# Kernel optimization log

Measured on AMD Instinct MI355X. Metric: run time of the kernel, lower is better.

Reference implementation:

```python
import jax, jax.numpy as jnp
import numpy as np

NEG = -9e15

def setup_inputs() -> dict:
    key = jax.random.key(0)
    k_h, k_adj, k_W, k_bW, k_a1, k_b1, k_a2, k_b2 = jax.random.split(key, 8)
    N, IN, OUT = 8192, 512, 512
    h = jax.random.normal(k_h, (N, IN), dtype=jnp.float32)
    adj = jax.random.randint(k_adj, (N, N), 0, 2, dtype=jnp.int32)
    # torch Linear default init: U(-1/sqrt(fan_in), 1/sqrt(fan_in))
    s_in = 1.0 / np.sqrt(IN)
    s_out = 1.0 / np.sqrt(OUT)
    W = jax.random.uniform(k_W, (IN, OUT), minval=-s_in, maxval=s_in, dtype=jnp.float32)
    bW = jax.random.uniform(k_bW, (OUT,), minval=-s_in, maxval=s_in, dtype=jnp.float32)
    a1 = jax.random.uniform(k_a1, (OUT,), minval=-s_out, maxval=s_out, dtype=jnp.float32)
    b1 = jax.random.uniform(k_b1, (), minval=-s_out, maxval=s_out, dtype=jnp.float32)
    a2 = jax.random.uniform(k_a2, (OUT,), minval=-s_out, maxval=s_out, dtype=jnp.float32)
    b2 = jax.random.uniform(k_b2, (), minval=-s_out, maxval=s_out, dtype=jnp.float32)
    return {"h": h, "adj": adj, "W": W, "bW": bW, "a1": a1, "b1": b1, "a2": a2, "b2": b2}

def reference(h, adj, W, bW, a1, b1, a2, b2):
    alpha = 0.2
    # Wh: [N, OUT]; dropout is identity at inference (training=False)
    Wh = h @ W + bW
    Wha1 = Wh @ a1 + b1  # [N]
    Wha2 = Wh @ a2 + b2  # [N]
    e = Wha1[:, None] + Wha2[None, :]  # [N, N] broadcast additive scores
    e = jnp.where(e > 0, e, alpha * e)  # leaky relu
    e = jnp.where(adj > 0, e, jnp.float32(-9e15))
    attention = jax.nn.softmax(e, axis=1)
    h_prime = attention @ Wh  # [N, OUT]
    return h_prime
```

## Files before the change

kernel.cpp:

```cpp
#include <hip/hip_runtime.h>
#include <stdint.h>


#define NN 8192
#define DD 512

typedef __attribute__((ext_vector_type(8))) short short8;
typedef __attribute__((ext_vector_type(4))) float f32x4;
typedef __attribute__((ext_vector_type(4))) float float4v;
typedef __attribute__((ext_vector_type(4))) unsigned short ushort4v;

__device__ __forceinline__ uint16_t f2bf(float f) {
  union { float f; uint32_t u; } v; v.f = f;
  uint32_t u = v.u;
  u += 0x7fffu + ((u >> 16) & 1u);
  return (uint16_t)(u >> 16);
}
__device__ __forceinline__ float bf2f(uint16_t b) {
  union { uint32_t u; float f; } v; v.u = ((uint32_t)b) << 16;
  return v.f;
}

__device__ __forceinline__ void async_copy16(uint16_t* lds, const uint16_t* g) {
  __builtin_amdgcn_global_load_lds(
      (const __attribute__((address_space(1))) uint32_t*)g,
      (__attribute__((address_space(3))) uint32_t*)lds, 16, 0, 0);
}

__global__ __launch_bounds__(256) void conv_wt(const float* __restrict__ W,
                                               uint16_t* __restrict__ WT) {
  int idx = blockIdx.x * 256 + threadIdx.x;
  int k = idx >> 9, c = idx & 511;
  WT[c * 512 + k] = f2bf(W[idx]);
}

__global__ __launch_bounds__(512) void wh_gemm(const float* __restrict__ h,
                                               const uint16_t* __restrict__ WT,
                                               const float* __restrict__ bW,
                                               uint16_t* __restrict__ WhT) {
  __shared__ __align__(16) uint16_t At[32 * 32];
  __shared__ __align__(16) uint16_t Bt[512 * 32];
  int tid = threadIdx.x;
  int wave = tid >> 6, lane = tid & 63;
  int l15 = lane & 15, quad = lane >> 4;
  int i0 = blockIdx.x * 32;
  f32x4 acc[2][4] = {};
  for (int k0 = 0; k0 < 512; k0 += 32) {
    if (tid < 256) {
      int r = tid >> 3, ks = (tid & 7) * 4;
      float4v hv = *(const float4v*)(h + (size_t)(i0 + r) * 512 + k0 + ks);
      ushort4v p;
      p.x = f2bf(hv.x); p.y = f2bf(hv.y); p.z = f2bf(hv.z); p.w = f2bf(hv.w);
      *(ushort4v*)&At[r * 32 + ks] = p;
    }
    #pragma unroll
    for (int rr = 0; rr < 4; ++rr) {
      int idx = rr * 512 + tid;
      int c = idx >> 2, q = idx & 3;
      async_copy16(&Bt[idx * 8], WT + c * 512 + k0 + q * 8);
    }
    __syncthreads();
    short8 a0 = *(const short8*)&At[l15 * 32 + quad * 8];
    short8 a1f = *(const short8*)&At[(l15 + 16) * 32 + quad * 8];
    #pragma unroll
    for (int nt = 0; nt < 4; ++nt) {
      int c = wave * 64 + nt * 16 + l15;
      short8 b = *(const short8*)&Bt[c * 32 + quad * 8];
      acc[0][nt] = __builtin_amdgcn_mfma_f32_16x16x32_bf16(a0, b, acc[0][nt], 0, 0, 0);
      acc[1][nt] = __builtin_amdgcn_mfma_f32_16x16x32_bf16(a1f, b, acc[1][nt], 0, 0, 0);
    }
    __syncthreads();
  }
  #pragma unroll
  for (int mt = 0; mt < 2; ++mt) {
    int ib = i0 + mt * 16 + quad * 4;
    #pragma unroll
    for (int nt = 0; nt < 4; ++nt) {
      int c = wave * 64 + nt * 16 + l15;
      float bias = bW[c];
      ushort4v p;
      p.x = f2bf(acc[mt][nt].x + bias);
      p.y = f2bf(acc[mt][nt].y + bias);
      p.z = f2bf(acc[mt][nt].z + bias);
      p.w = f2bf(acc[mt][nt].w + bias);
      *(ushort4v*)&WhT[(size_t)c * 8192 + ib] = p;
    }
  }
}

__global__ __launch_bounds__(256) void zero_k(float* __restrict__ p) {
  p[blockIdx.x * 256 + threadIdx.x] = 0.f;
}

__global__ __launch_bounds__(256) void scores2(const uint16_t* __restrict__ WhT,
                                               const float* __restrict__ a1,
                                               const float* __restrict__ a2,
                                               float* __restrict__ s1,
                                               float* __restrict__ s2) {
  int cc = blockIdx.x >> 5;
  int ic = blockIdx.x & 31;
  int i = ic * 256 + threadIdx.x;
  float r1 = 0.f, r2 = 0.f;
  int cbase = cc * 128;
  #pragma unroll 8
  for (int c = cbase; c < cbase + 128; ++c) {
    float v = bf2f(WhT[(size_t)c * 8192 + i]);
    r1 = fmaf(v, a1[c], r1);
    r2 = fmaf(v, a2[c], r2);
  }
  atomicAdd(&s1[i], r1);
  atomicAdd(&s2[i], r2);
}

__global__ __launch_bounds__(256) void w_k(const int* __restrict__ adj,
                                           const float* __restrict__ s1,
                                           const float* __restrict__ s2,
                                           const float* __restrict__ b1,
                                           const float* __restrict__ b2,
                                           uint16_t* __restrict__ w,
                                           float* __restrict__ dinv) {
  __shared__ float wsum[4];
  int i = blockIdx.x;
  int tid = threadIdx.x;
  float base = s1[i] + b1[0] + b2[0];
  const int* arow = adj + (size_t)i * 8192;
  uint16_t* wrow = w + (size_t)i * 8192;
  float sum = 0.f;
  #pragma unroll
  for (int it = 0; it < 8; ++it) {
    int j = it * 1024 + tid * 4;
    int4 av = *(const int4*)(arow + j);
    float4v sv = *(const float4v*)(s2 + j);
    float e, wv;
    ushort4v p;
    e = base + sv.x; e = fmaxf(e, 0.2f * e);
    wv = (av.x > 0) ? __expf(e) : 0.f; p.x = f2bf(wv); sum += bf2f(p.x);
    e = base + sv.y; e = fmaxf(e, 0.2f * e);
    wv = (av.y > 0) ? __expf(e) : 0.f; p.y = f2bf(wv); sum += bf2f(p.y);
    e = base + sv.z; e = fmaxf(e, 0.2f * e);
    wv = (av.z > 0) ? __expf(e) : 0.f; p.z = f2bf(wv); sum += bf2f(p.z);
    e = base + sv.w; e = fmaxf(e, 0.2f * e);
    wv = (av.w > 0) ? __expf(e) : 0.f; p.w = f2bf(wv); sum += bf2f(p.w);
    *(ushort4v*)(wrow + j) = p;
  }
  #pragma unroll
  for (int o = 32; o > 0; o >>= 1) sum += __shfl_down(sum, o);
  if ((tid & 63) == 0) wsum[tid >> 6] = sum;
  __syncthreads();
  if (tid == 0) dinv[i] = 1.0f / (wsum[0] + wsum[1] + wsum[2] + wsum[3]);
}

__global__ __launch_bounds__(512, 4) void pv_gemm(const uint16_t* __restrict__ w,
                                                  const uint16_t* __restrict__ WhT,
                                                  const float* __restrict__ dinv,
                                                  float* __restrict__ out) {
  __shared__ __align__(16) uint16_t At[64 * 64];
  __shared__ __align__(16) uint16_t Bt[128 * 64];
  __shared__ float sdv[64];
  int tid = threadIdx.x;
  int wave = tid >> 6, lane = tid & 63;
  int l15 = lane & 15, quad = lane >> 4;
  int rb = blockIdx.x >> 2, cb = blockIdx.x & 3;
  int i0 = rb * 64, c0 = cb * 128;
  if (tid < 64) sdv[tid] = dinv[i0 + tid];
  f32x4 acc[4] = {};
  int arow = tid >> 3, acp = tid & 7;
  int acc_chunk = acp ^ (arow & 7);
  for (int j0 = 0; j0 < 8192; j0 += 64) {
    async_copy16(&At[tid * 8],
                 w + (size_t)(i0 + arow) * 8192 + j0 + acc_chunk * 8);
    #pragma unroll
    for (int k = 0; k < 2; ++k) {
      int bidx = k * 512 + tid;
      int br = bidx >> 3, bcp = bidx & 7;
      int bcc = bcp ^ (br & 7);
      async_copy16(&Bt[bidx * 8],
                   WhT + (size_t)(c0 + br) * 8192 + j0 + bcc * 8);
    }
    __syncthreads();
    #pragma unroll
    for (int ks = 0; ks < 2; ++ks) {
      int bro = wave * 16 + l15;
      short8 b = *(const short8*)&Bt[bro * 64 + (((ks * 4 + quad) ^ (bro & 7)) * 8)];
      #pragma unroll
      for (int rt = 0; rt < 4; ++rt) {
        int aro = rt * 16 + l15;
        short8 a = *(const short8*)&At[aro * 64 + (((ks * 4 + quad) ^ (aro & 7)) * 8)];
        acc[rt] = __builtin_amdgcn_mfma_f32_16x16x32_bf16(a, b, acc[rt], 0, 0, 0);
      }
    }
    __syncthreads();
  }
  #pragma unroll
  for (int rt = 0; rt < 4; ++rt) {
    #pragma unroll
    for (int v = 0; v < 4; ++v) {
      int rloc = rt * 16 + quad * 4 + v;
      out[(size_t)(i0 + rloc) * 512 + c0 + wave * 16 + l15] = acc[rt][v] * sdv[rloc];
    }
  }
}

__global__ __launch_bounds__(256) void scores_k(const uint16_t* __restrict__ WhT,
                                                const float* __restrict__ a1,
                                                const float* __restrict__ b1,
                                                const float* __restrict__ a2,
                                                const float* __restrict__ b2,
                                                float* __restrict__ s1,
                                                float* __restrict__ s2) {
  int i = blockIdx.x * 256 + threadIdx.x;
  float r1 = 0.f, r2 = 0.f;
  #pragma unroll 8
  for (int c = 0; c < 512; ++c) {
    float v = bf2f(WhT[(size_t)c * 8192 + i]);
    r1 = fmaf(v, a1[c], r1);
    r2 = fmaf(v, a2[c], r2);
  }
  s1[i] = r1 + b1[0];
  s2[i] = r2 + b2[0];
}

__global__ __launch_bounds__(512) void attn_k(const int* __restrict__ adj,
                                              const float* __restrict__ s1,
                                              const float* __restrict__ s2,
                                              const uint16_t* __restrict__ WhT,
                                              float* __restrict__ out) {
  __shared__ __align__(16) uint16_t At[32 * 32];
  __shared__ __align__(16) uint16_t Bt[512 * 32];
  __shared__ float dred[512];
  __shared__ float dinv[32];
  int tid = threadIdx.x;
  int wave = tid >> 6, lane = tid & 63;
  int l15 = lane & 15, quad = lane >> 4;
  int i0 = blockIdx.x * 32;
  int wr = tid >> 4;
  int wc = (tid & 15) * 2;
  float s1v = s1[i0 + wr];
  float dpart = 0.f;
  f32x4 acc[2][4] = {};
  const int* adjrow = adj + (size_t)(i0 + wr) * 8192 + wc;
  for (int j0 = 0; j0 < 8192; j0 += 32) {
    int2 av = *(const int2*)(adjrow + j0);
    float2 s2v = *(const float2*)(s2 + j0 + wc);
    float e0 = s1v + s2v.x; e0 = fmaxf(e0, 0.2f * e0);
    float e1 = s1v + s2v.y; e1 = fmaxf(e1, 0.2f * e1);
    float w0 = (av.x > 0) ? __expf(e0) : 0.f;
    float w1 = (av.y > 0) ? __expf(e1) : 0.f;
    dpart += w0 + w1;
    uint32_t packed = (uint32_t)f2bf(w0) | ((uint32_t)f2bf(w1) << 16);
    *(uint32_t*)&At[wr * 32 + wc] = packed;
    #pragma unroll
    for (int rr = 0; rr < 4; ++rr) {
      int idx = rr * 512 + tid;
      int c = idx >> 2, q = idx & 3;
      async_copy16(&Bt[idx * 8], WhT + (size_t)c * 8192 + j0 + q * 8);
    }
    __syncthreads();
    short8 a0 = *(const short8*)&At[l15 * 32 + quad * 8];
    short8 a1f = *(const short8*)&At[(l15 + 16) * 32 + quad * 8];
    #pragma unroll
    for (int nt = 0; nt < 4; ++nt) {
      short8 b = *(const short8*)&Bt[(wave * 64 + nt * 16 + l15) * 32 + quad * 8];
      acc[0][nt] = __builtin_amdgcn_mfma_f32_16x16x32_bf16(a0, b, acc[0][nt], 0, 0, 0);
      acc[1][nt] = __builtin_amdgcn_mfma_f32_16x16x32_bf16(a1f, b, acc[1][nt], 0, 0, 0);
    }
    __syncthreads();
  }
  dred[tid] = dpart;
  __syncthreads();
  if (tid < 32) {
    float s = 0.f;
    #pragma unroll
    for (int q = 0; q < 16; ++q) s += dred[tid * 16 + q];
    dinv[tid] = 1.0f / s;
  }
  __syncthreads();
  #pragma unroll
  for (int mt = 0; mt < 2; ++mt) {
    #pragma unroll
    for (int nt = 0; nt < 4; ++nt) {
      int c = wave * 64 + nt * 16 + l15;
      #pragma unroll
      for (int v = 0; v < 4; ++v) {
        int row = mt * 16 + quad * 4 + v;
        out[(size_t)(i0 + row) * 512 + c] = acc[mt][nt][v] * dinv[row];
      }
    }
  }
}

extern "C" void kernel_launch(void* const* d_in, const int* in_sizes, int n_in,
                              void* d_out, int out_size, void* d_ws, size_t ws_size,
                              hipStream_t stream) {
  const float* h   = (const float*)d_in[0];
  const int*   adj = (const int*)d_in[1];
  const float* W   = (const float*)d_in[2];
  const float* bW  = (const float*)d_in[3];
  const float* a1  = (const float*)d_in[4];
  const float* b1  = (const float*)d_in[5];
  const float* a2  = (const float*)d_in[6];
  const float* b2  = (const float*)d_in[7];
  float* out = (float*)d_out;
  char* ws = (char*)d_ws;

  const size_t NEED = 143228928ULL;
  if (ws_size >= NEED) {
    uint16_t* w   = (uint16_t*)(ws);
    uint16_t* WhT = (uint16_t*)(ws + 134217728);
    uint16_t* WT  = (uint16_t*)(ws + 142606336);
    float* s1     = (float*)(ws + 143130624);
    float* s2     = (float*)(ws + 143163392);
    float* dinv   = (float*)(ws + 143196160);

    conv_wt<<<1024, 256, 0, stream>>>(W, WT);
    wh_gemm<<<256, 512, 0, stream>>>(h, WT, bW, WhT);
    zero_k<<<64, 256, 0, stream>>>(s1);
    scores2<<<128, 256, 0, stream>>>(WhT, a1, a2, s1, s2);
    w_k<<<8192, 256, 0, stream>>>(adj, s1, s2, b1, b2, w, dinv);
    pv_gemm<<<512, 512, 0, stream>>>(w, WhT, dinv, out);
  } else {
    uint16_t* WhT = (uint16_t*)(ws);
    uint16_t* WT  = (uint16_t*)(ws + 8388608);
    float* s1     = (float*)(ws + 8912896);
    float* s2     = (float*)(ws + 8945664);

    conv_wt<<<1024, 256, 0, stream>>>(W, WT);
    wh_gemm<<<256, 512, 0, stream>>>(h, WT, bW, WhT);
    scores_k<<<32, 256, 0, stream>>>(WhT, a1, b1, a2, b2, s1, s2);
    attn_k<<<256, 512, 0, stream>>>(adj, s1, s2, WhT, out);
  }
}
```

Before: 567.7 us.

## Fuse score reductions into Wh GEMM, tile W transpose, deepen PV GEMM K-tile

```diff
diff --git a/kernel.cpp b/kernel.cpp
--- a/kernel.cpp
+++ b/kernel.cpp
@@ -29,21 +29,45 @@
 
 __global__ __launch_bounds__(256) void conv_wt(const float* __restrict__ W,
                                                uint16_t* __restrict__ WT) {
-  int idx = blockIdx.x * 256 + threadIdx.x;
-  int k = idx >> 9, c = idx & 511;
-  WT[c * 512 + k] = f2bf(W[idx]);
+  __shared__ float ts[64][65];
+  int tid = threadIdx.x;
+  int kt = (blockIdx.x >> 3) * 64, ct = (blockIdx.x & 7) * 64;
+  #pragma unroll
+  for (int it = 0; it < 4; ++it) {
+    int idx = it * 256 + tid;
+    int r = idx >> 4, q = idx & 15;
+    float4v v = *(const float4v*)(W + (size_t)(kt + r) * 512 + ct + q * 4);
+    ts[r][q * 4 + 0] = v.x; ts[r][q * 4 + 1] = v.y;
+    ts[r][q * 4 + 2] = v.z; ts[r][q * 4 + 3] = v.w;
+  }
+  __syncthreads();
+  #pragma unroll
+  for (int it = 0; it < 4; ++it) {
+    int idx = it * 256 + tid;
+    int c = idx >> 4, q = idx & 15;
+    ushort4v p;
+    p.x = f2bf(ts[q * 4 + 0][c]); p.y = f2bf(ts[q * 4 + 1][c]);
+    p.z = f2bf(ts[q * 4 + 2][c]); p.w = f2bf(ts[q * 4 + 3][c]);
+    *(ushort4v*)(WT + (size_t)(ct + c) * 512 + kt + q * 4) = p;
+  }
 }
 
 __global__ __launch_bounds__(512) void wh_gemm(const float* __restrict__ h,
                                                const uint16_t* __restrict__ WT,
                                                const float* __restrict__ bW,
-                                               uint16_t* __restrict__ WhT) {
+                                               const float* __restrict__ a1,
+                                               const float* __restrict__ a2,
+                                               uint16_t* __restrict__ WhT,
+                                               float* __restrict__ s1g,
+                                               float* __restrict__ s2g) {
   __shared__ __align__(16) uint16_t At[32 * 32];
   __shared__ __align__(16) uint16_t Bt[512 * 32];
+  __shared__ float s1loc[32], s2loc[32];
   int tid = threadIdx.x;
   int wave = tid >> 6, lane = tid & 63;
   int l15 = lane & 15, quad = lane >> 4;
   int i0 = blockIdx.x * 32;
+  if (tid < 32) { s1loc[tid] = 0.f; s2loc[tid] = 0.f; }
   f32x4 acc[2][4] = {};
   for (int k0 = 0; k0 < 512; k0 += 32) {
     if (tid < 256) {
@@ -74,42 +98,37 @@
   #pragma unroll
   for (int mt = 0; mt < 2; ++mt) {
     int ib = i0 + mt * 16 + quad * 4;
+    float r1[4] = {0.f, 0.f, 0.f, 0.f};
+    float r2[4] = {0.f, 0.f, 0.f, 0.f};
     #pragma unroll
     for (int nt = 0; nt < 4; ++nt) {
       int c = wave * 64 + nt * 16 + l15;
       float bias = bW[c];
+      float a1c = a1[c], a2c = a2[c];
+      float v0 = acc[mt][nt].x + bias;
+      float v1 = acc[mt][nt].y + bias;
+      float v2 = acc[mt][nt].z + bias;
+      float v3 = acc[mt][nt].w + bias;
       ushort4v p;
-      p.x = f2bf(acc[mt][nt].x + bias);
-      p.y = f2bf(acc[mt][nt].y + bias);
-      p.z = f2bf(acc[mt][nt].z + bias);
-      p.w = f2bf(acc[mt][nt].w + bias);
+      p.x = f2bf(v0); p.y = f2bf(v1); p.z = f2bf(v2); p.w = f2bf(v3);
       *(ushort4v*)&WhT[(size_t)c * 8192 + ib] = p;
-    }
-  }
-}
-
-__global__ __launch_bounds__(256) void zero_k(float* __restrict__ p) {
-  p[blockIdx.x * 256 + threadIdx.x] = 0.f;
-}
-
-__global__ __launch_bounds__(256) void scores2(const uint16_t* __restrict__ WhT,
-                                               const float* __restrict__ a1,
-                                               const float* __restrict__ a2,
-                                               float* __restrict__ s1,
-                                               float* __restrict__ s2) {
-  int cc = blockIdx.x >> 5;
-  int ic = blockIdx.x & 31;
-  int i = ic * 256 + threadIdx.x;
-  float r1 = 0.f, r2 = 0.f;
-  int cbase = cc * 128;
-  #pragma unroll 8
-  for (int c = cbase; c < cbase + 128; ++c) {
-    float v = bf2f(WhT[(size_t)c * 8192 + i]);
-    r1 = fmaf(v, a1[c], r1);
-    r2 = fmaf(v, a2[c], r2);
-  }
-  atomicAdd(&s1[i], r1);
-  atomicAdd(&s2[i], r2);
+      r1[0] = fmaf(v0, a1c, r1[0]); r1[1] = fmaf(v1, a1c, r1[1]);
+      r1[2] = fmaf(v2, a1c, r1[2]); r1[3] = fmaf(v3, a1c, r1[3]);
+      r2[0] = fmaf(v0, a2c, r2[0]); r2[1] = fmaf(v1, a2c, r2[1]);
+      r2[2] = fmaf(v2, a2c, r2[2]); r2[3] = fmaf(v3, a2c, r2[3]);
+    }
+    #pragma unroll
+    for (int v = 0; v < 4; ++v) {
+      int row = mt * 16 + quad * 4 + v;
+      atomicAdd(&s1loc[row], r1[v]);
+      atomicAdd(&s2loc[row], r2[v]);
+    }
+  }
+  __syncthreads();
+  if (tid < 32) {
+    s1g[i0 + tid] = s1loc[tid];
+    s2g[i0 + tid] = s2loc[tid];
+  }
 }
 
 __global__ __launch_bounds__(256) void w_k(const int* __restrict__ adj,
@@ -154,38 +173,41 @@
                                                   const uint16_t* __restrict__ WhT,
                                                   const float* __restrict__ dinv,
                                                   float* __restrict__ out) {
-  __shared__ __align__(16) uint16_t At[64 * 64];
-  __shared__ __align__(16) uint16_t Bt[128 * 64];
+  __shared__ __align__(16) uint16_t At[64 * 128];
+  __shared__ __align__(16) uint16_t Bt[128 * 128];
   __shared__ float sdv[64];
   int tid = threadIdx.x;
   int wave = tid >> 6, lane = tid & 63;
   int l15 = lane & 15, quad = lane >> 4;
-  int rb = blockIdx.x >> 2, cb = blockIdx.x & 3;
+  int rb = blockIdx.x & 127, cb = blockIdx.x >> 7;
   int i0 = rb * 64, c0 = cb * 128;
   if (tid < 64) sdv[tid] = dinv[i0 + tid];
   f32x4 acc[4] = {};
-  int arow = tid >> 3, acp = tid & 7;
-  int acc_chunk = acp ^ (arow & 7);
-  for (int j0 = 0; j0 < 8192; j0 += 64) {
-    async_copy16(&At[tid * 8],
-                 w + (size_t)(i0 + arow) * 8192 + j0 + acc_chunk * 8);
-    #pragma unroll
-    for (int k = 0; k < 2; ++k) {
-      int bidx = k * 512 + tid;
-      int br = bidx >> 3, bcp = bidx & 7;
-      int bcc = bcp ^ (br & 7);
-      async_copy16(&Bt[bidx * 8],
-                   WhT + (size_t)(c0 + br) * 8192 + j0 + bcc * 8);
-    }
-    __syncthreads();
-    #pragma unroll
-    for (int ks = 0; ks < 2; ++ks) {
-      int bro = wave * 16 + l15;
-      short8 b = *(const short8*)&Bt[bro * 64 + (((ks * 4 + quad) ^ (bro & 7)) * 8)];
+  for (int j0 = 0; j0 < 8192; j0 += 128) {
+    #pragma unroll
+    for (int it = 0; it < 2; ++it) {
+      int idx = it * 512 + tid;
+      int r = idx >> 4, p = idx & 15;
+      int sc = p ^ (r & 15);
+      async_copy16(&At[idx * 8], w + (size_t)(i0 + r) * 8192 + j0 + sc * 8);
+    }
+    #pragma unroll
+    for (int it = 0; it < 4; ++it) {
+      int idx = it * 512 + tid;
+      int r = idx >> 4, p = idx & 15;
+      int sc = p ^ (r & 15);
+      async_copy16(&Bt[idx * 8], WhT + (size_t)(c0 + r) * 8192 + j0 + sc * 8);
+    }
+    __syncthreads();
+    int brow = wave * 16 + l15;
+    #pragma unroll
+    for (int ks = 0; ks < 4; ++ks) {
+      int ch = ks * 4 + quad;
+      short8 b = *(const short8*)&Bt[brow * 128 + ((ch ^ (brow & 15)) * 8)];
       #pragma unroll
       for (int rt = 0; rt < 4; ++rt) {
-        int aro = rt * 16 + l15;
-        short8 a = *(const short8*)&At[aro * 64 + (((ks * 4 + quad) ^ (aro & 7)) * 8)];
+        int arow = rt * 16 + l15;
+        short8 a = *(const short8*)&At[arow * 128 + ((ch ^ (arow & 15)) * 8)];
         acc[rt] = __builtin_amdgcn_mfma_f32_16x16x32_bf16(a, b, acc[rt], 0, 0, 0);
       }
     }
@@ -201,28 +223,11 @@
   }
 }
 
-__global__ __launch_bounds__(256) void scores_k(const uint16_t* __restrict__ WhT,
-                                                const float* __restrict__ a1,
-                                                const float* __restrict__ b1,
-                                                const float* __restrict__ a2,
-                                                const float* __restrict__ b2,
-                                                float* __restrict__ s1,
-                                                float* __restrict__ s2) {
-  int i = blockIdx.x * 256 + threadIdx.x;
-  float r1 = 0.f, r2 = 0.f;
-  #pragma unroll 8
-  for (int c = 0; c < 512; ++c) {
-    float v = bf2f(WhT[(size_t)c * 8192 + i]);
-    r1 = fmaf(v, a1[c], r1);
-    r2 = fmaf(v, a2[c], r2);
-  }
-  s1[i] = r1 + b1[0];
-  s2[i] = r2 + b2[0];
-}
-
 __global__ __launch_bounds__(512) void attn_k(const int* __restrict__ adj,
                                               const float* __restrict__ s1,
                                               const float* __restrict__ s2,
+                                              const float* __restrict__ b1,
+                                              const float* __restrict__ b2,
                                               const uint16_t* __restrict__ WhT,
                                               float* __restrict__ out) {
   __shared__ __align__(16) uint16_t At[32 * 32];
@@ -235,7 +240,7 @@
   int i0 = blockIdx.x * 32;
   int wr = tid >> 4;
   int wc = (tid & 15) * 2;
-  float s1v = s1[i0 + wr];
+  float s1v = s1[i0 + wr] + b1[0] + b2[0];
   float dpart = 0.f;
   f32x4 acc[2][4] = {};
   const int* adjrow = adj + (size_t)(i0 + wr) * 8192 + wc;
@@ -312,10 +317,8 @@
     float* s2     = (float*)(ws + 143163392);
     float* dinv   = (float*)(ws + 143196160);
 
-    conv_wt<<<1024, 256, 0, stream>>>(W, WT);
-    wh_gemm<<<256, 512, 0, stream>>>(h, WT, bW, WhT);
-    zero_k<<<64, 256, 0, stream>>>(s1);
-    scores2<<<128, 256, 0, stream>>>(WhT, a1, a2, s1, s2);
+    conv_wt<<<64, 256, 0, stream>>>(W, WT);
+    wh_gemm<<<256, 512, 0, stream>>>(h, WT, bW, a1, a2, WhT, s1, s2);
     w_k<<<8192, 256, 0, stream>>>(adj, s1, s2, b1, b2, w, dinv);
     pv_gemm<<<512, 512, 0, stream>>>(w, WhT, dinv, out);
   } else {
@@ -324,9 +327,8 @@
     float* s1     = (float*)(ws + 8912896);
     float* s2     = (float*)(ws + 8945664);
 
-    conv_wt<<<1024, 256, 0, stream>>>(W, WT);
-    wh_gemm<<<256, 512, 0, stream>>>(h, WT, bW, WhT);
-    scores_k<<<32, 256, 0, stream>>>(WhT, a1, b1, a2, b2, s1, s2);
-    attn_k<<<256, 512, 0, stream>>>(adj, s1, s2, WhT, out);
-  }
-}
+    conv_wt<<<64, 256, 0, stream>>>(W, WT);
+    wh_gemm<<<256, 512, 0, stream>>>(h, WT, bW, a1, a2, WhT, s1, s2);
+    attn_k<<<256, 512, 0, stream>>>(adj, s1, s2, b1, b2, WhT, out);
+  }
+}
```

New measurement: 537.5 us. 5.3% less time.
